# Optimization experiments

Hardware: AMD Instinct MI355X
Metric: run time of the kernel (lower is better)

## Reference

```python
import jax, jax.numpy as jnp
import numpy as np

EPS = 1e-6

def _l2norm(x):
    # torch F.normalize(dim=1): x / max(||x||_2, eps), norm over channel axis 1
    n = jnp.sqrt(jnp.sum(x * x, axis=1, keepdims=True))
    return x / jnp.maximum(n, EPS)

def setup_inputs() -> dict:
    key = jax.random.key(0)
    ks = jax.random.split(key, 8)
    B, C, Cenc, dk, dv, H, W = 2, 320, 326, 64, 64, 64, 64
    return {
        "x": jax.random.normal(ks[0], (B, C, H, W), jnp.float32),
        "x_enc": jax.random.normal(ks[1], (B, Cenc, H, W), jnp.float32),
        "Wq": jax.random.normal(ks[2], (dk, Cenc), jnp.float32) * 0.05,
        "bq": jnp.zeros((dk,), jnp.float32),
        "Wk": jax.random.normal(ks[3], (dk, Cenc), jnp.float32) * 0.05,
        "bk": jnp.zeros((dk,), jnp.float32),
        "Wv": jax.random.normal(ks[4], (dv, C), jnp.float32) * 0.05,
        "bv": jnp.zeros((dv,), jnp.float32),
    }

def reference(x, x_enc, Wq, bq, Wk, bk, Wv, bv):
    B, C, H, Wd = x.shape
    L = H * Wd
    xe = x_enc.reshape(B, x_enc.shape[1], L)   # [B, Cenc, L]
    xf = x.reshape(B, C, L)                    # [B, C, L]
    # 1x1 conv projections == channel matmuls
    Q = jnp.einsum('oc,bcl->bol', Wq, xe) + bq[None, :, None]  # [B, dk, L]
    K = jnp.einsum('oc,bcl->bol', Wk, xe) + bk[None, :, None]  # [B, dk, L]
    V = jnp.einsum('oc,bcl->bol', Wv, xf) + bv[None, :, None]  # [B, dv, L]
    # cosine (L2-normalized) attention
    Qn = _l2norm(Q)
    Kn = _l2norm(K)
    A = jax.nn.softmax(jnp.einsum('bqi,bqj->bij', Qn, Kn), axis=-1)  # [B, L, L]
    R = jnp.einsum('bij,bvj->bvi', A, V)       # [B, dv, L]
    return R.reshape(B, V.shape[1], H, Wd)
```

## Files before the change

kernel.cpp:

```cpp
#include <hip/hip_runtime.h>


#define L_DIM 4096
#define KPAD 384
#define NSPLIT 8

typedef __attribute__((ext_vector_type(8))) short bf16x8;
typedef __attribute__((ext_vector_type(4))) float f32x4;

__device__ __forceinline__ unsigned short f2bf(float f) {
    unsigned u = __float_as_uint(f);
    u += 0x7fffu + ((u >> 16) & 1u);
    return (unsigned short)(u >> 16);
}

__device__ __forceinline__ float bf2f(unsigned short h) {
    return __uint_as_float((unsigned)h << 16);
}

__global__ __launch_bounds__(256) void prep_kernel(
    const float* __restrict__ x, const float* __restrict__ xe,
    const float* __restrict__ Wq, const float* __restrict__ Wk,
    const float* __restrict__ Wv,
    unsigned short* __restrict__ xt_x, unsigned short* __restrict__ xt_xe,
    unsigned short* __restrict__ wbf)
{
    const int z = blockIdx.z;
    if (z == 4) {
        const int bid = blockIdx.y * 64 + blockIdx.x;
        const int idx = bid * 256 + threadIdx.x;
        if (idx >= 3 * 64 * KPAD) return;
        const int t = idx / (64 * KPAD);
        const int rem = idx - t * 64 * KPAD;
        const int d = rem / KPAD, c = rem - d * KPAD;
        const int Cin = (t == 2) ? 320 : 326;
        const float* W = (t == 0) ? Wq : (t == 1 ? Wk : Wv);
        wbf[idx] = (c < Cin) ? f2bf(W[(size_t)d * Cin + c]) : (unsigned short)0;
        return;
    }

    const int src_is_x = z >> 1, b = z & 1;
    const int c0 = blockIdx.y * 64;
    const int l0 = blockIdx.x * 64;
    const int Cin = src_is_x ? 320 : 326;
    const float* src = (src_is_x ? x : xe) + (size_t)b * Cin * L_DIM;
    unsigned short* dst = (src_is_x ? xt_x : xt_xe) + (size_t)b * L_DIM * KPAD;

    __shared__ float tile[64][65];
    const int tid = threadIdx.x;

    #pragma unroll
    for (int it = 0; it < 4; ++it) {
        const int idx = tid + it * 256;
        const int cc = idx >> 4, lq = idx & 15;
        const int c = c0 + cc;
        float4 v = make_float4(0.f, 0.f, 0.f, 0.f);
        if (c < Cin) v = *(const float4*)(src + (size_t)c * L_DIM + l0 + lq * 4);
        tile[cc][lq * 4 + 0] = v.x;
        tile[cc][lq * 4 + 1] = v.y;
        tile[cc][lq * 4 + 2] = v.z;
        tile[cc][lq * 4 + 3] = v.w;
    }
    __syncthreads();
    #pragma unroll
    for (int it = 0; it < 4; ++it) {
        const int idx = tid + it * 256;
        const int ll = idx >> 4, cq = idx & 15;
        ushort4 o;
        o.x = f2bf(tile[cq * 4 + 0][ll]);
        o.y = f2bf(tile[cq * 4 + 1][ll]);
        o.z = f2bf(tile[cq * 4 + 2][ll]);
        o.w = f2bf(tile[cq * 4 + 3][ll]);
        *(ushort4*)(dst + (size_t)(l0 + ll) * KPAD + c0 + cq * 4) = o;
    }
}

__global__ __launch_bounds__(128) void proj_kernel(
    const unsigned short* __restrict__ xt_xe, const unsigned short* __restrict__ xt_x,
    const unsigned short* __restrict__ wbf,
    const float* __restrict__ bq, const float* __restrict__ bk,
    const float* __restrict__ bv,
    unsigned short* __restrict__ qn, unsigned short* __restrict__ kn,
    unsigned short* __restrict__ vbf)
{
    const int z = blockIdx.y;
    const int tensor = z >> 1, b = z & 1;
    const int l0 = blockIdx.x * 64;
    const int tid = threadIdx.x;
    const int w = tid >> 6, lane = tid & 63;
    const int q = lane >> 4, ln = lane & 15;

    const unsigned short* Xt = (tensor == 2 ? xt_x : xt_xe) + (size_t)b * L_DIM * KPAD;
    const unsigned short* W  = wbf + (size_t)tensor * 64 * KPAD;
    const float* bias = (tensor == 0) ? bq : (tensor == 1 ? bk : bv);

    __shared__ float red[64][68];

    f32x4 acc[4][4];
    #pragma unroll
    for (int mf = 0; mf < 4; ++mf)
        #pragma unroll
        for (int nf = 0; nf < 4; ++nf) acc[mf][nf] = (f32x4){0.f, 0.f, 0.f, 0.f};

    const int kbase = w * 6 * 32;

    bf16x8 af[4], bfr[4], afn[4], bfn[4];
    #pragma unroll
    for (int mf = 0; mf < 4; ++mf)
        af[mf] = *(const bf16x8*)(W + (size_t)(mf * 16 + ln) * KPAD + kbase + q * 8);
    #pragma unroll
    for (int nf = 0; nf < 4; ++nf)
        bfr[nf] = *(const bf16x8*)(Xt + (size_t)(l0 + nf * 16 + ln) * KPAD + kbase + q * 8);

    for (int ks = 0; ks < 6; ++ks) {
        if (ks + 1 < 6) {
            const int c = kbase + (ks + 1) * 32 + q * 8;
            #pragma unroll
            for (int mf = 0; mf < 4; ++mf)
                afn[mf] = *(const bf16x8*)(W + (size_t)(mf * 16 + ln) * KPAD + c);
            #pragma unroll
            for (int nf = 0; nf < 4; ++nf)
                bfn[nf] = *(const bf16x8*)(Xt + (size_t)(l0 + nf * 16 + ln) * KPAD + c);
        }
        #pragma unroll
        for (int mf = 0; mf < 4; ++mf)
            #pragma unroll
            for (int nf = 0; nf < 4; ++nf)
                acc[mf][nf] = __builtin_amdgcn_mfma_f32_16x16x32_bf16(
                    af[mf], bfr[nf], acc[mf][nf], 0, 0, 0);
        #pragma unroll
        for (int mf = 0; mf < 4; ++mf) af[mf] = afn[mf];
        #pragma unroll
        for (int nf = 0; nf < 4; ++nf) bfr[nf] = bfn[nf];
    }

    if (w == 1) {
        #pragma unroll
        for (int mf = 0; mf < 4; ++mf)
            #pragma unroll
            for (int nf = 0; nf < 4; ++nf)
                *(f32x4*)&red[lane][(mf * 4 + nf) * 4] = acc[mf][nf];
    }
    __syncthreads();
    if (w != 0) return;

    #pragma unroll
    for (int mf = 0; mf < 4; ++mf)
        #pragma unroll
        for (int nf = 0; nf < 4; ++nf) {
            const f32x4 p = *(const f32x4*)&red[lane][(mf * 4 + nf) * 4];
            acc[mf][nf] += p;
        }

    #pragma unroll
    for (int mf = 0; mf < 4; ++mf)
        #pragma unroll
        for (int r = 0; r < 4; ++r) {
            const float bb = bias[mf * 16 + q * 4 + r];
            #pragma unroll
            for (int nf = 0; nf < 4; ++nf) acc[mf][nf][r] += bb;
        }

    if (tensor < 2) {
        unsigned short* outp = (tensor ? kn : qn) + (size_t)b * L_DIM * 64;
        #pragma unroll
        for (int nf = 0; nf < 4; ++nf) {
            float s = 0.f;
            #pragma unroll
            for (int mf = 0; mf < 4; ++mf)
                #pragma unroll
                for (int r = 0; r < 4; ++r) s += acc[mf][nf][r] * acc[mf][nf][r];
            s += __shfl_xor(s, 16);
            s += __shfl_xor(s, 32);
            const float rn = 1.0f / fmaxf(sqrtf(s), 1e-6f);
            const size_t lrow = (size_t)(l0 + nf * 16 + ln) * 64;
            #pragma unroll
            for (int mf = 0; mf < 4; ++mf) {
                ushort4 o;
                o.x = f2bf(acc[mf][nf][0] * rn);
                o.y = f2bf(acc[mf][nf][1] * rn);
                o.z = f2bf(acc[mf][nf][2] * rn);
                o.w = f2bf(acc[mf][nf][3] * rn);
                *(ushort4*)(outp + lrow + mf * 16 + q * 4) = o;
            }
        }
    } else {
        unsigned short* outp = vbf + (size_t)b * 64 * L_DIM;
        #pragma unroll
        for (int mf = 0; mf < 4; ++mf)
            #pragma unroll
            for (int r = 0; r < 4; ++r) {
                const int v = mf * 16 + q * 4 + r;
                #pragma unroll
                for (int nf = 0; nf < 4; ++nf)
                    outp[(size_t)v * L_DIM + l0 + nf * 16 + ln] = f2bf(acc[mf][nf][r]);
            }
    }
}

__global__ __launch_bounds__(256) void attn_kernel(
    const unsigned short* __restrict__ qn, const unsigned short* __restrict__ kn,
    const unsigned short* __restrict__ vbf,
    unsigned short* __restrict__ opart, float* __restrict__ ssum)
{
    const int b = blockIdx.z, split = blockIdx.y;
    const int i0 = blockIdx.x * 128;
    const int tid = threadIdx.x;
    const int w = tid >> 6, lane = tid & 63, q = lane >> 4, ln = lane & 15;

    const unsigned short* Q = qn + (size_t)b * L_DIM * 64;
    const unsigned short* K = kn + (size_t)b * L_DIM * 64;
    const unsigned short* V = vbf + (size_t)b * 64 * L_DIM;

    __shared__ unsigned short Kb[64][72];
    __shared__ unsigned short Vb[64][72];
    __shared__ unsigned short Pl[4][32][72];

    bf16x8 qa[2][2];
    #pragma unroll
    for (int s = 0; s < 2; ++s) {
        const unsigned short* qp = Q + (size_t)(i0 + w * 32 + s * 16 + ln) * 64 + q * 8;
        qa[s][0] = *(const bf16x8*)(qp);
        qa[s][1] = *(const bf16x8*)(qp + 32);
    }

    f32x4 acc[2][4];
    #pragma unroll
    for (int s = 0; s < 2; ++s)
        #pragma unroll
        for (int vf = 0; vf < 4; ++vf) acc[s][vf] = (f32x4){0.f, 0.f, 0.f, 0.f};
    float rowsum[2] = {0.f, 0.f};
    const f32x4 zero = (f32x4){0.f, 0.f, 0.f, 0.f};

    const int jbase = split * (L_DIM / NSPLIT);
    const int JT = L_DIM / (NSPLIT * 64);

    bf16x8 kst[2], vst[2];
    #pragma unroll
    for (int p = 0; p < 2; ++p) {
        const int idx = p * 256 + tid;
        kst[p] = *(const bf16x8*)(K + (size_t)jbase * 64 + idx * 8);
        vst[p] = *(const bf16x8*)(V + (size_t)(idx >> 3) * L_DIM + jbase + (idx & 7) * 8);
    }
    #pragma unroll
    for (int p = 0; p < 2; ++p) {
        const int idx = p * 256 + tid;
        *(bf16x8*)&Kb[idx >> 3][(idx & 7) * 8] = kst[p];
        *(bf16x8*)&Vb[idx >> 3][(idx & 7) * 8] = vst[p];
    }
    __syncthreads();

    for (int jt = 0; jt < JT; ++jt) {
        if (jt + 1 < JT) {
            const int j0 = jbase + (jt + 1) * 64;
            #pragma unroll
            for (int p = 0; p < 2; ++p) {
                const int idx = p * 256 + tid;
                kst[p] = *(const bf16x8*)(K + (size_t)j0 * 64 + idx * 8);
                vst[p] = *(const bf16x8*)(V + (size_t)(idx >> 3) * L_DIM + j0 + (idx & 7) * 8);
            }
        }

        bf16x8 kf[4][2];
        #pragma unroll
        for (int jf = 0; jf < 4; ++jf) {
            kf[jf][0] = *(const bf16x8*)&Kb[jf * 16 + ln][q * 8];
            kf[jf][1] = *(const bf16x8*)&Kb[jf * 16 + ln][q * 8 + 32];
        }

        #pragma unroll
        for (int s = 0; s < 2; ++s) {
            #pragma unroll
            for (int jf = 0; jf < 4; ++jf) {
                f32x4 st;
                st = __builtin_amdgcn_mfma_f32_16x16x32_bf16(kf[jf][0], qa[s][0], zero, 0, 0, 0);
                st = __builtin_amdgcn_mfma_f32_16x16x32_bf16(kf[jf][1], qa[s][1], st, 0, 0, 0);
                const float p0 = __expf(st[0]);
                const float p1 = __expf(st[1]);
                const float p2 = __expf(st[2]);
                const float p3 = __expf(st[3]);
                rowsum[s] += (p0 + p1) + (p2 + p3);
                ushort4 pk;
                pk.x = f2bf(p0); pk.y = f2bf(p1); pk.z = f2bf(p2); pk.w = f2bf(p3);
                *(ushort4*)&Pl[w][s * 16 + ln][jf * 16 + q * 4] = pk;
            }
        }

        bf16x8 vfr[4][2];
        #pragma unroll
        for (int vf = 0; vf < 4; ++vf) {
            vfr[vf][0] = *(const bf16x8*)&Vb[vf * 16 + ln][q * 8];
            vfr[vf][1] = *(const bf16x8*)&Vb[vf * 16 + ln][q * 8 + 32];
        }

        #pragma unroll
        for (int s = 0; s < 2; ++s) {
            const bf16x8 pb0 = *(const bf16x8*)&Pl[w][s * 16 + ln][q * 8];
            const bf16x8 pb1 = *(const bf16x8*)&Pl[w][s * 16 + ln][q * 8 + 32];
            #pragma unroll
            for (int vf = 0; vf < 4; ++vf) {
                acc[s][vf] = __builtin_amdgcn_mfma_f32_16x16x32_bf16(vfr[vf][0], pb0, acc[s][vf], 0, 0, 0);
                acc[s][vf] = __builtin_amdgcn_mfma_f32_16x16x32_bf16(vfr[vf][1], pb1, acc[s][vf], 0, 0, 0);
            }
        }

        __syncthreads();
        if (jt + 1 < JT) {
            #pragma unroll
            for (int p = 0; p < 2; ++p) {
                const int idx = p * 256 + tid;
                *(bf16x8*)&Kb[idx >> 3][(idx & 7) * 8] = kst[p];
                *(bf16x8*)&Vb[idx >> 3][(idx & 7) * 8] = vst[p];
            }
            __syncthreads();
        }
    }

    #pragma unroll
    for (int s = 0; s < 2; ++s) {
        rowsum[s] += __shfl_xor(rowsum[s], 16);
        rowsum[s] += __shfl_xor(rowsum[s], 32);
    }

    unsigned short* Op = opart + ((size_t)(b * NSPLIT + split) * L_DIM + i0 + w * 32) * 64;
    #pragma unroll
    for (int s = 0; s < 2; ++s)
        #pragma unroll
        for (int vf = 0; vf < 4; ++vf) {
            ushort4 o;
            o.x = f2bf(acc[s][vf][0]); o.y = f2bf(acc[s][vf][1]);
            o.z = f2bf(acc[s][vf][2]); o.w = f2bf(acc[s][vf][3]);
            *(ushort4*)&Op[(s * 16 + ln) * 64 + vf * 16 + q * 4] = o;
        }

    if (q == 0) {
        #pragma unroll
        for (int s = 0; s < 2; ++s)
            ssum[(size_t)(b * NSPLIT + split) * L_DIM + i0 + w * 32 + s * 16 + ln]
                = rowsum[s];
    }
}

__global__ __launch_bounds__(256) void combine_kernel(
    const unsigned short* __restrict__ opart, const float* __restrict__ ssum,
    float* __restrict__ out)
{
    const int b = blockIdx.y;
    const int i0 = blockIdx.x * 64;
    const int tid = threadIdx.x;
    __shared__ float t[64][65];
    __shared__ float sinv[64];

    if (tid < 64) {
        float s = 0.f;
        for (int sp = 0; sp < NSPLIT; ++sp)
            s += ssum[(size_t)(b * NSPLIT + sp) * L_DIM + i0 + tid];
        sinv[tid] = 1.0f / s;
    }
    __syncthreads();
    for (int it = 0; it < 4; ++it) {
        const int idx = tid + it * 256;
        const int i = idx >> 4, vq = idx & 15;
        float a0 = 0.f, a1 = 0.f, a2 = 0.f, a3 = 0.f;
        for (int sp = 0; sp < NSPLIT; ++sp) {
            const ushort4 p = *(const ushort4*)&opart[
                (((size_t)(b * NSPLIT + sp) * L_DIM + i0 + i)) * 64 + vq * 4];
            a0 += bf2f(p.x); a1 += bf2f(p.y); a2 += bf2f(p.z); a3 += bf2f(p.w);
        }
        t[i][vq * 4 + 0] = a0;
        t[i][vq * 4 + 1] = a1;
        t[i][vq * 4 + 2] = a2;
        t[i][vq * 4 + 3] = a3;
    }
    __syncthreads();
    for (int idx = tid; idx < 4096; idx += 256) {
        const int v = idx >> 6, i = idx & 63;
        out[((size_t)(b * 64 + v)) * L_DIM + i0 + i] = t[i][v] * sinv[i];
    }
}

extern "C" void kernel_launch(void* const* d_in, const int* in_sizes, int n_in,
                              void* d_out, int out_size, void* d_ws, size_t ws_size,
                              hipStream_t stream)
{
    const float* x  = (const float*)d_in[0];
    const float* xe = (const float*)d_in[1];
    const float* Wq = (const float*)d_in[2];
    const float* bq = (const float*)d_in[3];
    const float* Wk = (const float*)d_in[4];
    const float* bk = (const float*)d_in[5];
    const float* Wv = (const float*)d_in[6];
    const float* bv = (const float*)d_in[7];
    float* out = (float*)d_out;

    char* ws = (char*)d_ws;
    unsigned short* qn   = (unsigned short*)(ws);
    unsigned short* kn   = (unsigned short*)(ws + (1u << 20));
    unsigned short* vbf  = (unsigned short*)(ws + (2u << 20));
    float*          ss   = (float*)(ws + (3u << 20));
    unsigned short* wb   = (unsigned short*)(ws + (3u << 20) + (512u << 10));
    unsigned short* xtxe = (unsigned short*)(ws + (4u << 20));
    unsigned short* xtx  = (unsigned short*)(ws + (10u << 20));
    unsigned short* op   = (unsigned short*)(ws + (16u << 20));

    prep_kernel<<<dim3(64, 6, 5), 256, 0, stream>>>(x, xe, Wq, Wk, Wv, xtx, xtxe, wb);
    proj_kernel<<<dim3(64, 6), 128, 0, stream>>>(xtxe, xtx, wb, bq, bk, bv, qn, kn, vbf);
    attn_kernel<<<dim3(32, NSPLIT, 2), 256, 0, stream>>>(qn, kn, vbf, op, ss);
    combine_kernel<<<dim3(64, 2), 256, 0, stream>>>(op, ss, out);
}
```

Baseline: 112.1 us.

## Load K and V fragments directly from global memory, dropping LDS staging

After: 126.1 us. 12.5% more time.

```diff
diff --git a/kernel.cpp b/kernel.cpp
--- a/kernel.cpp
+++ b/kernel.cpp
@@ -212,8 +212,6 @@
     const unsigned short* K = kn + (size_t)b * L_DIM * 64;
     const unsigned short* V = vbf + (size_t)b * 64 * L_DIM;
 
-    __shared__ unsigned short Kb[64][72];
-    __shared__ unsigned short Vb[64][72];
     __shared__ unsigned short Pl[4][32][72];
 
     bf16x8 qa[2][2];
@@ -235,37 +233,23 @@
     const int jbase = split * (L_DIM / NSPLIT);
     const int JT = L_DIM / (NSPLIT * 64);
 
-    bf16x8 kst[2], vst[2];
-    #pragma unroll
-    for (int p = 0; p < 2; ++p) {
-        const int idx = p * 256 + tid;
-        kst[p] = *(const bf16x8*)(K + (size_t)jbase * 64 + idx * 8);
-        vst[p] = *(const bf16x8*)(V + (size_t)(idx >> 3) * L_DIM + jbase + (idx & 7) * 8);
-    }
-    #pragma unroll
-    for (int p = 0; p < 2; ++p) {
-        const int idx = p * 256 + tid;
-        *(bf16x8*)&Kb[idx >> 3][(idx & 7) * 8] = kst[p];
-        *(bf16x8*)&Vb[idx >> 3][(idx & 7) * 8] = vst[p];
-    }
-    __syncthreads();
-
     for (int jt = 0; jt < JT; ++jt) {
-        if (jt + 1 < JT) {
-            const int j0 = jbase + (jt + 1) * 64;
-            #pragma unroll
-            for (int p = 0; p < 2; ++p) {
-                const int idx = p * 256 + tid;
-                kst[p] = *(const bf16x8*)(K + (size_t)j0 * 64 + idx * 8);
-                vst[p] = *(const bf16x8*)(V + (size_t)(idx >> 3) * L_DIM + j0 + (idx & 7) * 8);
-            }
-        }
+        const int j0 = jbase + jt * 64;
 
         bf16x8 kf[4][2];
         #pragma unroll
         for (int jf = 0; jf < 4; ++jf) {
-            kf[jf][0] = *(const bf16x8*)&Kb[jf * 16 + ln][q * 8];
-            kf[jf][1] = *(const bf16x8*)&Kb[jf * 16 + ln][q * 8 + 32];
+            const unsigned short* kp = K + (size_t)(j0 + jf * 16 + ln) * 64 + q * 8;
+            kf[jf][0] = *(const bf16x8*)(kp);
+            kf[jf][1] = *(const bf16x8*)(kp + 32);
+        }
+
+        bf16x8 vfr[4][2];
+        #pragma unroll
+        for (int vf = 0; vf < 4; ++vf) {
+            const unsigned short* vp = V + (size_t)(vf * 16 + ln) * L_DIM + j0 + q * 8;
+            vfr[vf][0] = *(const bf16x8*)(vp);
+            vfr[vf][1] = *(const bf16x8*)(vp + 32);
         }
 
         #pragma unroll
@@ -286,13 +270,6 @@
             }
         }
 
-        bf16x8 vfr[4][2];
-        #pragma unroll
-        for (int vf = 0; vf < 4; ++vf) {
-            vfr[vf][0] = *(const bf16x8*)&Vb[vf * 16 + ln][q * 8];
-            vfr[vf][1] = *(const bf16x8*)&Vb[vf * 16 + ln][q * 8 + 32];
-        }
-
         #pragma unroll
         for (int s = 0; s < 2; ++s) {
             const bf16x8 pb0 = *(const bf16x8*)&Pl[w][s * 16 + ln][q * 8];
@@ -302,17 +279,6 @@
                 acc[s][vf] = __builtin_amdgcn_mfma_f32_16x16x32_bf16(vfr[vf][0], pb0, acc[s][vf], 0, 0, 0);
                 acc[s][vf] = __builtin_amdgcn_mfma_f32_16x16x32_bf16(vfr[vf][1], pb1, acc[s][vf], 0, 0, 0);
             }
-        }
-
-        __syncthreads();
-        if (jt + 1 < JT) {
-            #pragma unroll
-            for (int p = 0; p < 2; ++p) {
-                const int idx = p * 256 + tid;
-                *(bf16x8*)&Kb[idx >> 3][(idx & 7) * 8] = kst[p];
-                *(bf16x8*)&Vb[idx >> 3][(idx & 7) * 8] = vst[p];
-            }
-            __syncthreads();
         }
     }
 
```
